# Performance work log

Hardware: AMD Instinct MI355X
Metric: run time of the kernel (lower is better)

## Reference

```python
import jax, jax.numpy as jnp
import numpy as np

N = 200000   # nodes
E = 6400000  # edges
F = 128      # input node features
H = 6        # hiddenSize (module constant)
C = 10       # num_classes
G = 64       # graphs in batch


def setup_inputs() -> dict:
    key = jax.random.key(0)
    ks = jax.random.split(key, 7)
    x = jax.random.normal(ks[0], (N, F), dtype=jnp.float32)
    edge_index = jax.random.randint(ks[1], (2, E), 0, N, dtype=jnp.int32)
    batch = jnp.sort(jax.random.randint(ks[2], (N,), 0, G, dtype=jnp.int32))
    W1 = jax.random.normal(ks[3], (F, H), dtype=jnp.float32) * (1.0 / np.sqrt(F))
    b1 = jnp.zeros((H,), dtype=jnp.float32)
    W2 = jax.random.normal(ks[4], (H, C), dtype=jnp.float32) * (1.0 / np.sqrt(H))
    b2 = jnp.zeros((C,), dtype=jnp.float32)
    return {"x": x, "edge_index": edge_index, "batch": batch,
            "W1": W1, "b1": b1, "W2": W2, "b2": b2}


def _gcn_conv(x, W, b, row, col, dis):
    # PyG GCNConv: h = x W; out = D^{-1/2}(A+I)D^{-1/2} h + b
    h = x @ W                                      # [N, out]
    norm = dis[row] * dis[col]                     # [E] edge normalization
    msg = norm[:, None] * h[row]                   # gather from source nodes
    agg = jax.ops.segment_sum(msg, col, num_segments=N)  # scatter-add to targets
    # self-loop term: norm = dis[i]*dis[i]
    return agg + (dis * dis)[:, None] * h + b


def reference(x, edge_index, batch, W1, b1, W2, b2):
    row, col = edge_index[0], edge_index[1]
    # degree after adding self-loops (edge_weight = 1)
    deg = jax.ops.segment_sum(jnp.ones((E,), dtype=x.dtype), col, num_segments=N) + 1.0
    dis = jax.lax.rsqrt(deg)                       # deg^{-1/2}

    h = _gcn_conv(x, W1, b1, row, col, dis)
    h = jax.nn.relu(h)
    # dropout is identity in inference mode
    h = _gcn_conv(h, W2, b2, row, col, dis)        # [N, C]

    # global mean pool over each graph
    sums = jax.ops.segment_sum(h, batch, num_segments=G)                  # [G, C]
    cnts = jax.ops.segment_sum(jnp.ones((N,), dtype=h.dtype), batch, num_segments=G)
    pooled = sums / jnp.maximum(cnts, 1.0)[:, None]
    return jax.nn.log_softmax(pooled, axis=1)      # [G, C]
```

## Files before the change

### kernel.cpp

```cpp
#include <hip/hip_runtime.h>
#include <math.h>

#define N_NODES 200000
#define N_EDGES 6400000
#define F_IN    128
#define H_HID   6
#define C_OUT   10
#define G_BATCH 64

#define TILE_E  16384
#define NT      ((N_EDGES + TILE_E - 1) / TILE_E)
#define NBUCK   ((N_NODES + 1023) / 1024)
#define BCAP    36864
#define EPT     (TILE_E / 512)
#define QCAP    10240

__device__ __forceinline__ unsigned short f2bf(float f) {
    unsigned u = __float_as_uint(f);
    u += 0x7fff + ((u >> 16) & 1);
    return (unsigned short)(u >> 16);
}
__device__ __forceinline__ unsigned pack2(float a, float b) {
    return (unsigned)f2bf(a) | ((unsigned)f2bf(b) << 16);
}
__device__ __forceinline__ float bf_lo(unsigned u) { return __uint_as_float(u << 16); }
__device__ __forceinline__ float bf_hi(unsigned u) { return __uint_as_float(u & 0xffff0000u); }

__global__ __launch_bounds__(512) void scatterA_kernel(const int* __restrict__ row,
                                                       const int* __restrict__ col,
                                                       int* __restrict__ gcur,
                                                       int* __restrict__ binned, int E) {
    __shared__ int sortbuf[TILE_E];
    __shared__ int cnt[256];
    __shared__ int pos[257];
    __shared__ int cur[256];
    __shared__ int lbase[256];
    int t = blockIdx.x, tid = threadIdx.x;
    int base = t * TILE_E;
    int tile_n = min(TILE_E, E - base);

    if (tid < 256) cnt[tid] = 0;
    __syncthreads();

    int myval[EPT];
#pragma unroll
    for (int k = 0; k < EPT; ++k) {
        int e = base + k * 512 + tid;
        if (e < E) {
            int c = col[e];
            myval[k] = ((c & 1023) << 18) | row[e];
            atomicAdd(&cnt[c >> 10], 1);
        }
    }
    __syncthreads();

    if (tid < 256) pos[tid] = cnt[tid];
    __syncthreads();
    for (int off = 1; off < 256; off <<= 1) {
        int tv = (tid < 256 && tid >= off) ? pos[tid - off] : 0;
        __syncthreads();
        if (tid < 256) pos[tid] += tv;
        __syncthreads();
    }
    int incl = (tid < 256) ? pos[tid] : 0;
    __syncthreads();
    if (tid < 256) {
        int excl = incl - cnt[tid];
        pos[tid] = excl;
        cur[tid] = excl;
        if (tid == 255) pos[256] = incl;
        if (tid < NBUCK) {
            int c = cnt[tid];
            lbase[tid] = tid * BCAP + (c ? atomicAdd(&gcur[tid], c) : 0);
        }
    }
    __syncthreads();

#pragma unroll
    for (int k = 0; k < EPT; ++k) {
        int e = base + k * 512 + tid;
        if (e < E) {
            int b = col[e] >> 10;
            int p = atomicAdd(&cur[b], 1);
            sortbuf[p] = myval[k];
        }
    }
    __syncthreads();

    for (int i = tid; i < tile_n; i += 512) {
        int lo = 0, hi = NBUCK - 1;
        while (lo < hi) {
            int mid = (lo + hi + 1) >> 1;
            if (pos[mid] <= i) lo = mid; else hi = mid - 1;
        }
        binned[lbase[lo] + (i - pos[lo])] = sortbuf[i];
    }
}

__global__ __launch_bounds__(1024) void passB_kernel(const int* __restrict__ gcur,
                                                     const int* __restrict__ binned,
                                                     int* __restrict__ offs, int* __restrict__ endo,
                                                     float* __restrict__ dis,
                                                     int* __restrict__ csr, int E) {
    __shared__ int cnt[1024];
    __shared__ int scn[1024];
    __shared__ int cur[256];
    __shared__ int sortbuf[QCAP];
    int b = blockIdx.x, tid = threadIdx.x;
    int bb = b * BCAP;
    int be = bb + gcur[b];
    cnt[tid] = 0;
    __syncthreads();
    int e = bb + tid;
    for (; e + 3072 < be; e += 4096) {
        int p0 = binned[e], p1 = binned[e + 1024], p2 = binned[e + 2048], p3 = binned[e + 3072];
        atomicAdd(&cnt[p0 >> 18], 1); atomicAdd(&cnt[p1 >> 18], 1);
        atomicAdd(&cnt[p2 >> 18], 1); atomicAdd(&cnt[p3 >> 18], 1);
    }
    for (; e < be; e += 1024) atomicAdd(&cnt[binned[e] >> 18], 1);
    __syncthreads();
    int v = cnt[tid];
    scn[tid] = v;
    __syncthreads();
    for (int off = 1; off < 1024; off <<= 1) {
        int t2 = (tid >= off) ? scn[tid - off] : 0;
        __syncthreads();
        scn[tid] += t2;
        __syncthreads();
    }
    int excl = scn[tid] - v;
    scn[tid] = excl;
    int n = (b << 10) + tid;
    if (n < N_NODES) {
        offs[n] = bb + excl;
        endo[n] = bb + excl + v;
        dis[n] = rsqrtf((float)v + 1.0f);
    }
    __syncthreads();
    int total = be - bb;
#define PLACE(p) { int loc = (p) >> 18; if ((loc >> 8) == q) {                      \
        int ps = scn[loc] - qbase + atomicAdd(&cur[loc & 255], 1);                  \
        if (ps < QCAP) sortbuf[ps] = (p) & 0x3FFFF;                                 \
        else csr[bb + qbase + ps] = (p) & 0x3FFFF; } }
    for (int q = 0; q < 4; ++q) {
        int qbase = scn[q << 8];
        int qend = (q < 3) ? scn[(q + 1) << 8] : total;
        int qn = qend - qbase;
        if (tid < 256) cur[tid] = 0;
        __syncthreads();
        int e2 = bb + tid;
        for (; e2 + 3072 < be; e2 += 4096) {
            int p0 = binned[e2], p1 = binned[e2 + 1024], p2 = binned[e2 + 2048], p3 = binned[e2 + 3072];
            PLACE(p0) PLACE(p1) PLACE(p2) PLACE(p3)
        }
        for (; e2 < be; e2 += 1024) { int p = binned[e2]; PLACE(p) }
        __syncthreads();
        int lim = qn < QCAP ? qn : QCAP;
        for (int i = tid; i < lim; i += 1024) csr[bb + qbase + i] = sortbuf[i];
        __syncthreads();
    }
#undef PLACE
}

__global__ void xw1_kernel(const float* __restrict__ x, const float* __restrict__ W1,
                           const float* __restrict__ dis, uint4* __restrict__ h1b) {
    __shared__ float w[F_IN * H_HID];
    for (int i = threadIdx.x; i < F_IN * H_HID; i += blockDim.x) w[i] = W1[i];
    __syncthreads();
    int n = blockIdx.x * blockDim.x + threadIdx.x;
    if (n >= N_NODES) return;
    float acc[H_HID] = {0.f, 0.f, 0.f, 0.f, 0.f, 0.f};
    const float4* xr = (const float4*)(x + (size_t)n * F_IN);
#pragma unroll 4
    for (int f4 = 0; f4 < F_IN / 4; ++f4) {
        float4 v = xr[f4];
        int f = f4 * 4;
#pragma unroll
        for (int j = 0; j < H_HID; ++j) {
            acc[j] += v.x * w[(f + 0) * H_HID + j] + v.y * w[(f + 1) * H_HID + j]
                    + v.z * w[(f + 2) * H_HID + j] + v.w * w[(f + 3) * H_HID + j];
        }
    }
    float d = dis[n];
    uint4 o;
    o.x = pack2(d * acc[0], d * acc[1]);
    o.y = pack2(d * acc[2], d * acc[3]);
    o.z = pack2(d * acc[4], d * acc[5]);
    o.w = __float_as_uint(d);
    h1b[n] = o;
}

__global__ void gather1_kernel(const int* __restrict__ offs, const int* __restrict__ endo,
                               const int* __restrict__ csr,
                               const uint4* __restrict__ h1b, const float* __restrict__ b1,
                               uint4* __restrict__ rs) {
    int grp = threadIdx.x >> 3, sub = threadIdx.x & 7;
    int n = blockIdx.x * 32 + grp;
    int s = offs[n], e_end = endo[n];
    float a[H_HID] = {0.f, 0.f, 0.f, 0.f, 0.f, 0.f};
    int e = s + sub;
    for (; e + 24 < e_end; e += 32) {
        int i0 = csr[e], i1 = csr[e + 8], i2 = csr[e + 16], i3 = csr[e + 24];
        uint4 v0 = h1b[i0], v1 = h1b[i1], v2 = h1b[i2], v3 = h1b[i3];
        a[0] += (bf_lo(v0.x) + bf_lo(v1.x)) + (bf_lo(v2.x) + bf_lo(v3.x));
        a[1] += (bf_hi(v0.x) + bf_hi(v1.x)) + (bf_hi(v2.x) + bf_hi(v3.x));
        a[2] += (bf_lo(v0.y) + bf_lo(v1.y)) + (bf_lo(v2.y) + bf_lo(v3.y));
        a[3] += (bf_hi(v0.y) + bf_hi(v1.y)) + (bf_hi(v2.y) + bf_hi(v3.y));
        a[4] += (bf_lo(v0.z) + bf_lo(v1.z)) + (bf_lo(v2.z) + bf_lo(v3.z));
        a[5] += (bf_hi(v0.z) + bf_hi(v1.z)) + (bf_hi(v2.z) + bf_hi(v3.z));
    }
    for (; e < e_end; e += 8) {
        uint4 v = h1b[csr[e]];
        a[0] += bf_lo(v.x); a[1] += bf_hi(v.x);
        a[2] += bf_lo(v.y); a[3] += bf_hi(v.y);
        a[4] += bf_lo(v.z); a[5] += bf_hi(v.z);
    }
#pragma unroll
    for (int j = 0; j < H_HID; ++j)
#pragma unroll
        for (int off = 4; off > 0; off >>= 1) a[j] += __shfl_xor(a[j], off);
    uint4 self = h1b[n];
    float d = __uint_as_float(self.w);
    float sf[H_HID] = {bf_lo(self.x), bf_hi(self.x), bf_lo(self.y),
                       bf_hi(self.y), bf_lo(self.z), bf_hi(self.z)};
    if (sub == 0) {
        float r[H_HID];
#pragma unroll
        for (int j = 0; j < H_HID; ++j) {
            float vv = d * (a[j] + sf[j]) + b1[j];
            r[j] = d * (vv > 0.f ? vv : 0.f);
        }
        uint4 o;
        o.x = pack2(r[0], r[1]);
        o.y = pack2(r[2], r[3]);
        o.z = pack2(r[4], r[5]);
        o.w = self.w;
        rs[n] = o;
    }
}

__global__ void gather2_pool_kernel(const int* __restrict__ offs, const int* __restrict__ endo,
                                    const int* __restrict__ csr,
                                    const uint4* __restrict__ rs, const float* __restrict__ W2,
                                    const int* __restrict__ batch, float* __restrict__ sums) {
    __shared__ float w2s[H_HID * C_OUT];
    __shared__ float nodeval[32][C_OUT];
    __shared__ int lg[32];
    if (threadIdx.x < H_HID * C_OUT) w2s[threadIdx.x] = W2[threadIdx.x];
    __syncthreads();
    int grp = threadIdx.x >> 3, sub = threadIdx.x & 7;
    int n = blockIdx.x * 32 + grp;
    int s = offs[n], e_end = endo[n];
    float a[H_HID] = {0.f, 0.f, 0.f, 0.f, 0.f, 0.f};
    int e = s + sub;
    for (; e + 24 < e_end; e += 32) {
        int i0 = csr[e], i1 = csr[e + 8], i2 = csr[e + 16], i3 = csr[e + 24];
        uint4 v0 = rs[i0], v1 = rs[i1], v2 = rs[i2], v3 = rs[i3];
        a[0] += (bf_lo(v0.x) + bf_lo(v1.x)) + (bf_lo(v2.x) + bf_lo(v3.x));
        a[1] += (bf_hi(v0.x) + bf_hi(v1.x)) + (bf_hi(v2.x) + bf_hi(v3.x));
        a[2] += (bf_lo(v0.y) + bf_lo(v1.y)) + (bf_lo(v2.y) + bf_lo(v3.y));
        a[3] += (bf_hi(v0.y) + bf_hi(v1.y)) + (bf_hi(v2.y) + bf_hi(v3.y));
        a[4] += (bf_lo(v0.z) + bf_lo(v1.z)) + (bf_lo(v2.z) + bf_lo(v3.z));
        a[5] += (bf_hi(v0.z) + bf_hi(v1.z)) + (bf_hi(v2.z) + bf_hi(v3.z));
    }
    for (; e < e_end; e += 8) {
        uint4 v = rs[csr[e]];
        a[0] += bf_lo(v.x); a[1] += bf_hi(v.x);
        a[2] += bf_lo(v.y); a[3] += bf_hi(v.y);
        a[4] += bf_lo(v.z); a[5] += bf_hi(v.z);
    }
#pragma unroll
    for (int j = 0; j < H_HID; ++j)
#pragma unroll
        for (int off = 4; off > 0; off >>= 1) a[j] += __shfl_xor(a[j], off);
    uint4 self = rs[n];
    float d = __uint_as_float(self.w);
    float t[H_HID] = {a[0] + bf_lo(self.x), a[1] + bf_hi(self.x), a[2] + bf_lo(self.y),
                      a[3] + bf_hi(self.y), a[4] + bf_lo(self.z), a[5] + bf_hi(self.z)};
    {
        float acc = 0.f;
#pragma unroll
        for (int j = 0; j < H_HID; ++j) acc += t[j] * w2s[j * C_OUT + sub];
        nodeval[grp][sub] = d * acc;
        if (sub < 2) {
            float acc2 = 0.f;
#pragma unroll
            for (int j = 0; j < H_HID; ++j) acc2 += t[j] * w2s[j * C_OUT + sub + 8];
            nodeval[grp][sub + 8] = d * acc2;
        }
    }
    if (sub == 0) lg[grp] = batch[n];
    __syncthreads();
    if (threadIdx.x < C_OUT) {
        int c = threadIdx.x;
        float acc = 0.f;
        int gcur2 = lg[0];
#pragma unroll
        for (int w = 0; w < 32; ++w) {
            if (lg[w] != gcur2) {
                atomicAdd(&sums[gcur2 * C_OUT + c], acc);
                gcur2 = lg[w]; acc = 0.f;
            }
            acc += nodeval[w][c];
        }
        atomicAdd(&sums[gcur2 * C_OUT + c], acc);
    }
}

__global__ void pool_finish_kernel(const float* __restrict__ sums, const int* __restrict__ batch,
                                   const float* __restrict__ b2, float* __restrict__ out) {
    int g = threadIdx.x;
    if (g >= G_BATCH) return;
    int lo = 0, hi = N_NODES;
    while (lo < hi) { int mid = (lo + hi) >> 1; if (batch[mid] < g) lo = mid + 1; else hi = mid; }
    int c0 = lo;
    hi = N_NODES;
    while (lo < hi) { int mid = (lo + hi) >> 1; if (batch[mid] < g + 1) lo = mid + 1; else hi = mid; }
    float inv = 1.0f / fmaxf((float)(lo - c0), 1.0f);
    float v[C_OUT], m = -INFINITY;
#pragma unroll
    for (int c = 0; c < C_OUT; ++c) {
        v[c] = sums[g * C_OUT + c] * inv + b2[c];
        m = fmaxf(m, v[c]);
    }
    float s = 0.f;
#pragma unroll
    for (int c = 0; c < C_OUT; ++c) s += expf(v[c] - m);
    float lse = m + logf(s);
#pragma unroll
    for (int c = 0; c < C_OUT; ++c) out[g * C_OUT + c] = v[c] - lse;
}

extern "C" void kernel_launch(void* const* d_in, const int* in_sizes, int n_in,
                              void* d_out, int out_size, void* d_ws, size_t ws_size,
                              hipStream_t stream) {
    const float* x   = (const float*)d_in[0];
    const int* ei    = (const int*)d_in[1];
    const int* row   = ei;
    const int* col   = ei + N_EDGES;
    const int* batch = (const int*)d_in[2];
    const float* W1  = (const float*)d_in[3];
    const float* b1  = (const float*)d_in[4];
    const float* W2  = (const float*)d_in[5];
    const float* b2  = (const float*)d_in[6];
    float* out = (float*)d_out;

    char* p = (char*)d_ws;
    float* sums   = (float*)p;  p += (size_t)G_BATCH * C_OUT * 4;
    int*   gcur   = (int*)p;    p += (size_t)200 * 4;
    int*   offs   = (int*)p;    p += (size_t)N_NODES * 4;
    int*   endo   = (int*)p;    p += (size_t)N_NODES * 4;
    float* dis    = (float*)p;  p += (size_t)N_NODES * 4;
    int*   csr    = (int*)p;    p += (size_t)NBUCK * BCAP * 4;
    int*   binned = (int*)p;
    uint4* h1b    = (uint4*)binned;
    uint4* rs     = (uint4*)binned + N_NODES;

    hipMemsetAsync(sums, 0, (size_t)G_BATCH * C_OUT * 4 + 200 * 4, stream);

    scatterA_kernel<<<NT, 512, 0, stream>>>(row, col, gcur, binned, N_EDGES);
    passB_kernel   <<<NBUCK, 1024, 0, stream>>>(gcur, binned, offs, endo, dis, csr, N_EDGES);
    xw1_kernel     <<<(N_NODES + 255) / 256, 256, 0, stream>>>(x, W1, dis, h1b);
    gather1_kernel <<<N_NODES / 32, 256, 0, stream>>>(offs, endo, csr, h1b, b1, rs);
    gather2_pool_kernel<<<N_NODES / 32, 256, 0, stream>>>(offs, endo, csr, rs, W2, batch, sums);
    pool_finish_kernel <<<1, 64, 0, stream>>>(sums, batch, b2, out);
}
```

Before: 383.7 us.

## Replace CSR build with bucketed LDS atomic aggregation over 512-node bins

Drops the second sorting pass that turned bucketed edges into a per-node CSR. Both aggregation layers now run one block per 512-node bucket, gathering source features and adding them into per-bucket accumulators in shared memory with atomics. Degrees come from global atomics in the scatter pass, and the rsqrt normalisation is folded into the feature transform. This saves a full edge pass and the CSR arrays, but adds heavy LDS atomic contention (six float atomics per edge) and global degree atomics, and makes the summation order nondeterministic.

```diff
diff --git a/kernel.cpp b/kernel.cpp
--- a/kernel.cpp
+++ b/kernel.cpp
@@ -10,10 +10,11 @@
 
 #define TILE_E  16384
 #define NT      ((N_EDGES + TILE_E - 1) / TILE_E)
-#define NBUCK   ((N_NODES + 1023) / 1024)
-#define BCAP    36864
 #define EPT     (TILE_E / 512)
-#define QCAP    10240
+#define BSH     9
+#define BNODES  512
+#define NBUCK   ((N_NODES + BNODES - 1) / BNODES)
+#define BCAP    18432
 
 __device__ __forceinline__ unsigned short f2bf(float f) {
     unsigned u = __float_as_uint(f);
@@ -29,17 +30,18 @@
 __global__ __launch_bounds__(512) void scatterA_kernel(const int* __restrict__ row,
                                                        const int* __restrict__ col,
                                                        int* __restrict__ gcur,
+                                                       int* __restrict__ deg,
                                                        int* __restrict__ binned, int E) {
     __shared__ int sortbuf[TILE_E];
-    __shared__ int cnt[256];
-    __shared__ int pos[257];
-    __shared__ int cur[256];
-    __shared__ int lbase[256];
+    __shared__ int cnt[512];
+    __shared__ int pos[513];
+    __shared__ int cur[512];
+    __shared__ int lbase[512];
     int t = blockIdx.x, tid = threadIdx.x;
     int base = t * TILE_E;
     int tile_n = min(TILE_E, E - base);
 
-    if (tid < 256) cnt[tid] = 0;
+    cnt[tid] = 0;
     __syncthreads();
 
     int myval[EPT];
@@ -48,27 +50,28 @@
         int e = base + k * 512 + tid;
         if (e < E) {
             int c = col[e];
-            myval[k] = ((c & 1023) << 18) | row[e];
-            atomicAdd(&cnt[c >> 10], 1);
-        }
-    }
-    __syncthreads();
-
-    if (tid < 256) pos[tid] = cnt[tid];
-    __syncthreads();
-    for (int off = 1; off < 256; off <<= 1) {
-        int tv = (tid < 256 && tid >= off) ? pos[tid - off] : 0;
+            myval[k] = ((c & (BNODES - 1)) << 18) | row[e];
+            atomicAdd(&cnt[c >> BSH], 1);
+            atomicAdd(&deg[c], 1);
+        }
+    }
+    __syncthreads();
+
+    pos[tid] = cnt[tid];
+    __syncthreads();
+    for (int off = 1; off < 512; off <<= 1) {
+        int tv = (tid >= off) ? pos[tid - off] : 0;
         __syncthreads();
-        if (tid < 256) pos[tid] += tv;
+        pos[tid] += tv;
         __syncthreads();
     }
-    int incl = (tid < 256) ? pos[tid] : 0;
-    __syncthreads();
-    if (tid < 256) {
+    int incl = pos[tid];
+    __syncthreads();
+    {
         int excl = incl - cnt[tid];
         pos[tid] = excl;
         cur[tid] = excl;
-        if (tid == 255) pos[256] = incl;
+        if (tid == 511) pos[512] = incl;
         if (tid < NBUCK) {
             int c = cnt[tid];
             lbase[tid] = tid * BCAP + (c ? atomicAdd(&gcur[tid], c) : 0);
@@ -80,7 +83,7 @@
     for (int k = 0; k < EPT; ++k) {
         int e = base + k * 512 + tid;
         if (e < E) {
-            int b = col[e] >> 10;
+            int b = col[e] >> BSH;
             int p = atomicAdd(&cur[b], 1);
             sortbuf[p] = myval[k];
         }
@@ -97,73 +100,8 @@
     }
 }
 
-__global__ __launch_bounds__(1024) void passB_kernel(const int* __restrict__ gcur,
-                                                     const int* __restrict__ binned,
-                                                     int* __restrict__ offs, int* __restrict__ endo,
-                                                     float* __restrict__ dis,
-                                                     int* __restrict__ csr, int E) {
-    __shared__ int cnt[1024];
-    __shared__ int scn[1024];
-    __shared__ int cur[256];
-    __shared__ int sortbuf[QCAP];
-    int b = blockIdx.x, tid = threadIdx.x;
-    int bb = b * BCAP;
-    int be = bb + gcur[b];
-    cnt[tid] = 0;
-    __syncthreads();
-    int e = bb + tid;
-    for (; e + 3072 < be; e += 4096) {
-        int p0 = binned[e], p1 = binned[e + 1024], p2 = binned[e + 2048], p3 = binned[e + 3072];
-        atomicAdd(&cnt[p0 >> 18], 1); atomicAdd(&cnt[p1 >> 18], 1);
-        atomicAdd(&cnt[p2 >> 18], 1); atomicAdd(&cnt[p3 >> 18], 1);
-    }
-    for (; e < be; e += 1024) atomicAdd(&cnt[binned[e] >> 18], 1);
-    __syncthreads();
-    int v = cnt[tid];
-    scn[tid] = v;
-    __syncthreads();
-    for (int off = 1; off < 1024; off <<= 1) {
-        int t2 = (tid >= off) ? scn[tid - off] : 0;
-        __syncthreads();
-        scn[tid] += t2;
-        __syncthreads();
-    }
-    int excl = scn[tid] - v;
-    scn[tid] = excl;
-    int n = (b << 10) + tid;
-    if (n < N_NODES) {
-        offs[n] = bb + excl;
-        endo[n] = bb + excl + v;
-        dis[n] = rsqrtf((float)v + 1.0f);
-    }
-    __syncthreads();
-    int total = be - bb;
-#define PLACE(p) { int loc = (p) >> 18; if ((loc >> 8) == q) {                      \
-        int ps = scn[loc] - qbase + atomicAdd(&cur[loc & 255], 1);                  \
-        if (ps < QCAP) sortbuf[ps] = (p) & 0x3FFFF;                                 \
-        else csr[bb + qbase + ps] = (p) & 0x3FFFF; } }
-    for (int q = 0; q < 4; ++q) {
-        int qbase = scn[q << 8];
-        int qend = (q < 3) ? scn[(q + 1) << 8] : total;
-        int qn = qend - qbase;
-        if (tid < 256) cur[tid] = 0;
-        __syncthreads();
-        int e2 = bb + tid;
-        for (; e2 + 3072 < be; e2 += 4096) {
-            int p0 = binned[e2], p1 = binned[e2 + 1024], p2 = binned[e2 + 2048], p3 = binned[e2 + 3072];
-            PLACE(p0) PLACE(p1) PLACE(p2) PLACE(p3)
-        }
-        for (; e2 < be; e2 += 1024) { int p = binned[e2]; PLACE(p) }
-        __syncthreads();
-        int lim = qn < QCAP ? qn : QCAP;
-        for (int i = tid; i < lim; i += 1024) csr[bb + qbase + i] = sortbuf[i];
-        __syncthreads();
-    }
-#undef PLACE
-}
-
 __global__ void xw1_kernel(const float* __restrict__ x, const float* __restrict__ W1,
-                           const float* __restrict__ dis, uint4* __restrict__ h1b) {
+                           const int* __restrict__ deg, uint4* __restrict__ h1b) {
     __shared__ float w[F_IN * H_HID];
     for (int i = threadIdx.x; i < F_IN * H_HID; i += blockDim.x) w[i] = W1[i];
     __syncthreads();
@@ -181,7 +119,7 @@
                     + v.z * w[(f + 2) * H_HID + j] + v.w * w[(f + 3) * H_HID + j];
         }
     }
-    float d = dis[n];
+    float d = rsqrtf((float)deg[n] + 1.0f);
     uint4 o;
     o.x = pack2(d * acc[0], d * acc[1]);
     o.y = pack2(d * acc[2], d * acc[3]);
@@ -190,44 +128,47 @@
     h1b[n] = o;
 }
 
-__global__ void gather1_kernel(const int* __restrict__ offs, const int* __restrict__ endo,
-                               const int* __restrict__ csr,
-                               const uint4* __restrict__ h1b, const float* __restrict__ b1,
-                               uint4* __restrict__ rs) {
-    int grp = threadIdx.x >> 3, sub = threadIdx.x & 7;
-    int n = blockIdx.x * 32 + grp;
-    int s = offs[n], e_end = endo[n];
-    float a[H_HID] = {0.f, 0.f, 0.f, 0.f, 0.f, 0.f};
-    int e = s + sub;
-    for (; e + 24 < e_end; e += 32) {
-        int i0 = csr[e], i1 = csr[e + 8], i2 = csr[e + 16], i3 = csr[e + 24];
-        uint4 v0 = h1b[i0], v1 = h1b[i1], v2 = h1b[i2], v3 = h1b[i3];
-        a[0] += (bf_lo(v0.x) + bf_lo(v1.x)) + (bf_lo(v2.x) + bf_lo(v3.x));
-        a[1] += (bf_hi(v0.x) + bf_hi(v1.x)) + (bf_hi(v2.x) + bf_hi(v3.x));
-        a[2] += (bf_lo(v0.y) + bf_lo(v1.y)) + (bf_lo(v2.y) + bf_lo(v3.y));
-        a[3] += (bf_hi(v0.y) + bf_hi(v1.y)) + (bf_hi(v2.y) + bf_hi(v3.y));
-        a[4] += (bf_lo(v0.z) + bf_lo(v1.z)) + (bf_lo(v2.z) + bf_lo(v3.z));
-        a[5] += (bf_hi(v0.z) + bf_hi(v1.z)) + (bf_hi(v2.z) + bf_hi(v3.z));
-    }
-    for (; e < e_end; e += 8) {
-        uint4 v = h1b[csr[e]];
-        a[0] += bf_lo(v.x); a[1] += bf_hi(v.x);
-        a[2] += bf_lo(v.y); a[3] += bf_hi(v.y);
-        a[4] += bf_lo(v.z); a[5] += bf_hi(v.z);
-    }
-#pragma unroll
-    for (int j = 0; j < H_HID; ++j)
-#pragma unroll
-        for (int off = 4; off > 0; off >>= 1) a[j] += __shfl_xor(a[j], off);
-    uint4 self = h1b[n];
-    float d = __uint_as_float(self.w);
-    float sf[H_HID] = {bf_lo(self.x), bf_hi(self.x), bf_lo(self.y),
-                       bf_hi(self.y), bf_lo(self.z), bf_hi(self.z)};
-    if (sub == 0) {
+#define EDGE_ACC(v, l)                                                  \
+    atomicAdd(&acc[0][l], bf_lo(v.x)); atomicAdd(&acc[1][l], bf_hi(v.x)); \
+    atomicAdd(&acc[2][l], bf_lo(v.y)); atomicAdd(&acc[3][l], bf_hi(v.y)); \
+    atomicAdd(&acc[4][l], bf_lo(v.z)); atomicAdd(&acc[5][l], bf_hi(v.z));
+
+__global__ __launch_bounds__(512) void agg1_kernel(const int* __restrict__ gcur,
+                                                   const int* __restrict__ binned,
+                                                   const uint4* __restrict__ h1b,
+                                                   const float* __restrict__ b1,
+                                                   uint4* __restrict__ rs) {
+    __shared__ float acc[H_HID][BNODES];
+    int b = blockIdx.x, tid = threadIdx.x;
+#pragma unroll
+    for (int j = 0; j < H_HID; ++j) acc[j][tid] = 0.f;
+    __syncthreads();
+    int bb = b * BCAP, be = bb + gcur[b];
+    int e = bb + tid;
+    for (; e + 1536 < be; e += 2048) {
+        int p0 = binned[e], p1 = binned[e + 512], p2 = binned[e + 1024], p3 = binned[e + 1536];
+        uint4 v0 = h1b[p0 & 0x3FFFF], v1 = h1b[p1 & 0x3FFFF],
+              v2 = h1b[p2 & 0x3FFFF], v3 = h1b[p3 & 0x3FFFF];
+        int l0 = p0 >> 18, l1 = p1 >> 18, l2 = p2 >> 18, l3 = p3 >> 18;
+        EDGE_ACC(v0, l0) EDGE_ACC(v1, l1) EDGE_ACC(v2, l2) EDGE_ACC(v3, l3)
+    }
+    for (; e < be; e += 512) {
+        int p = binned[e];
+        uint4 v = h1b[p & 0x3FFFF];
+        int l = p >> 18;
+        EDGE_ACC(v, l)
+    }
+    __syncthreads();
+    int n = b * BNODES + tid;
+    if (n < N_NODES) {
+        uint4 self = h1b[n];
+        float d = __uint_as_float(self.w);
+        float sf[H_HID] = {bf_lo(self.x), bf_hi(self.x), bf_lo(self.y),
+                           bf_hi(self.y), bf_lo(self.z), bf_hi(self.z)};
         float r[H_HID];
 #pragma unroll
         for (int j = 0; j < H_HID; ++j) {
-            float vv = d * (a[j] + sf[j]) + b1[j];
+            float vv = d * (acc[j][tid] + sf[j]) + b1[j];
             r[j] = d * (vv > 0.f ? vv : 0.f);
         }
         uint4 o;
@@ -239,71 +180,71 @@
     }
 }
 
-__global__ void gather2_pool_kernel(const int* __restrict__ offs, const int* __restrict__ endo,
-                                    const int* __restrict__ csr,
-                                    const uint4* __restrict__ rs, const float* __restrict__ W2,
-                                    const int* __restrict__ batch, float* __restrict__ sums) {
+__global__ __launch_bounds__(512) void agg2_pool_kernel(const int* __restrict__ gcur,
+                                                        const int* __restrict__ binned,
+                                                        const uint4* __restrict__ rs,
+                                                        const float* __restrict__ W2,
+                                                        const int* __restrict__ batch,
+                                                        float* __restrict__ sums) {
+    __shared__ float acc[H_HID][BNODES];
     __shared__ float w2s[H_HID * C_OUT];
-    __shared__ float nodeval[32][C_OUT];
-    __shared__ int lg[32];
-    if (threadIdx.x < H_HID * C_OUT) w2s[threadIdx.x] = W2[threadIdx.x];
-    __syncthreads();
-    int grp = threadIdx.x >> 3, sub = threadIdx.x & 7;
-    int n = blockIdx.x * 32 + grp;
-    int s = offs[n], e_end = endo[n];
-    float a[H_HID] = {0.f, 0.f, 0.f, 0.f, 0.f, 0.f};
-    int e = s + sub;
-    for (; e + 24 < e_end; e += 32) {
-        int i0 = csr[e], i1 = csr[e + 8], i2 = csr[e + 16], i3 = csr[e + 24];
-        uint4 v0 = rs[i0], v1 = rs[i1], v2 = rs[i2], v3 = rs[i3];
-        a[0] += (bf_lo(v0.x) + bf_lo(v1.x)) + (bf_lo(v2.x) + bf_lo(v3.x));
-        a[1] += (bf_hi(v0.x) + bf_hi(v1.x)) + (bf_hi(v2.x) + bf_hi(v3.x));
-        a[2] += (bf_lo(v0.y) + bf_lo(v1.y)) + (bf_lo(v2.y) + bf_lo(v3.y));
-        a[3] += (bf_hi(v0.y) + bf_hi(v1.y)) + (bf_hi(v2.y) + bf_hi(v3.y));
-        a[4] += (bf_lo(v0.z) + bf_lo(v1.z)) + (bf_lo(v2.z) + bf_lo(v3.z));
-        a[5] += (bf_hi(v0.z) + bf_hi(v1.z)) + (bf_hi(v2.z) + bf_hi(v3.z));
-    }
-    for (; e < e_end; e += 8) {
-        uint4 v = rs[csr[e]];
-        a[0] += bf_lo(v.x); a[1] += bf_hi(v.x);
-        a[2] += bf_lo(v.y); a[3] += bf_hi(v.y);
-        a[4] += bf_lo(v.z); a[5] += bf_hi(v.z);
-    }
-#pragma unroll
-    for (int j = 0; j < H_HID; ++j)
-#pragma unroll
-        for (int off = 4; off > 0; off >>= 1) a[j] += __shfl_xor(a[j], off);
-    uint4 self = rs[n];
-    float d = __uint_as_float(self.w);
-    float t[H_HID] = {a[0] + bf_lo(self.x), a[1] + bf_hi(self.x), a[2] + bf_lo(self.y),
-                      a[3] + bf_hi(self.y), a[4] + bf_lo(self.z), a[5] + bf_hi(self.z)};
-    {
-        float acc = 0.f;
-#pragma unroll
-        for (int j = 0; j < H_HID; ++j) acc += t[j] * w2s[j * C_OUT + sub];
-        nodeval[grp][sub] = d * acc;
-        if (sub < 2) {
-            float acc2 = 0.f;
-#pragma unroll
-            for (int j = 0; j < H_HID; ++j) acc2 += t[j] * w2s[j * C_OUT + sub + 8];
-            nodeval[grp][sub + 8] = d * acc2;
-        }
-    }
-    if (sub == 0) lg[grp] = batch[n];
-    __syncthreads();
-    if (threadIdx.x < C_OUT) {
-        int c = threadIdx.x;
-        float acc = 0.f;
-        int gcur2 = lg[0];
-#pragma unroll
-        for (int w = 0; w < 32; ++w) {
-            if (lg[w] != gcur2) {
-                atomicAdd(&sums[gcur2 * C_OUT + c], acc);
-                gcur2 = lg[w]; acc = 0.f;
+    __shared__ float nv[BNODES][C_OUT + 1];
+    __shared__ int lg[BNODES];
+    int b = blockIdx.x, tid = threadIdx.x;
+#pragma unroll
+    for (int j = 0; j < H_HID; ++j) acc[j][tid] = 0.f;
+    if (tid < H_HID * C_OUT) w2s[tid] = W2[tid];
+    __syncthreads();
+    int bb = b * BCAP, be = bb + gcur[b];
+    int e = bb + tid;
+    for (; e + 1536 < be; e += 2048) {
+        int p0 = binned[e], p1 = binned[e + 512], p2 = binned[e + 1024], p3 = binned[e + 1536];
+        uint4 v0 = rs[p0 & 0x3FFFF], v1 = rs[p1 & 0x3FFFF],
+              v2 = rs[p2 & 0x3FFFF], v3 = rs[p3 & 0x3FFFF];
+        int l0 = p0 >> 18, l1 = p1 >> 18, l2 = p2 >> 18, l3 = p3 >> 18;
+        EDGE_ACC(v0, l0) EDGE_ACC(v1, l1) EDGE_ACC(v2, l2) EDGE_ACC(v3, l3)
+    }
+    for (; e < be; e += 512) {
+        int p = binned[e];
+        uint4 v = rs[p & 0x3FFFF];
+        int l = p >> 18;
+        EDGE_ACC(v, l)
+    }
+    __syncthreads();
+    int n = b * BNODES + tid;
+    if (n < N_NODES) {
+        uint4 self = rs[n];
+        float d = __uint_as_float(self.w);
+        float t0 = acc[0][tid] + bf_lo(self.x), t1 = acc[1][tid] + bf_hi(self.x),
+              t2 = acc[2][tid] + bf_lo(self.y), t3 = acc[3][tid] + bf_hi(self.y),
+              t4 = acc[4][tid] + bf_lo(self.z), t5 = acc[5][tid] + bf_hi(self.z);
+#pragma unroll
+        for (int c = 0; c < C_OUT; ++c) {
+            float a2 = t0 * w2s[c]             + t1 * w2s[C_OUT + c]
+                     + t2 * w2s[2 * C_OUT + c] + t3 * w2s[3 * C_OUT + c]
+                     + t4 * w2s[4 * C_OUT + c] + t5 * w2s[5 * C_OUT + c];
+            nv[tid][c] = d * a2;
+        }
+        lg[tid] = batch[n];
+    } else {
+#pragma unroll
+        for (int c = 0; c < C_OUT; ++c) nv[tid][c] = 0.f;
+        lg[tid] = G_BATCH - 1;
+    }
+    __syncthreads();
+    if (tid < 80) {
+        int seg = tid / 10, c = tid - seg * 10;
+        int g = -1; float a2 = 0.f;
+        for (int ii = 0; ii < 64; ++ii) {
+            int w = (seg << 6) + ((ii + 9 * seg) & 63);
+            int gw = lg[w];
+            if (gw != g) {
+                if (g >= 0) atomicAdd(&sums[g * C_OUT + c], a2);
+                g = gw; a2 = 0.f;
             }
-            acc += nodeval[w][c];
-        }
-        atomicAdd(&sums[gcur2 * C_OUT + c], acc);
+            a2 += nv[w][c];
+        }
+        atomicAdd(&sums[g * C_OUT + c], a2);
     }
 }
 
@@ -347,21 +288,18 @@
 
     char* p = (char*)d_ws;
     float* sums   = (float*)p;  p += (size_t)G_BATCH * C_OUT * 4;
-    int*   gcur   = (int*)p;    p += (size_t)200 * 4;
-    int*   offs   = (int*)p;    p += (size_t)N_NODES * 4;
-    int*   endo   = (int*)p;    p += (size_t)N_NODES * 4;
-    float* dis    = (float*)p;  p += (size_t)N_NODES * 4;
-    int*   csr    = (int*)p;    p += (size_t)NBUCK * BCAP * 4;
-    int*   binned = (int*)p;
-    uint4* h1b    = (uint4*)binned;
-    uint4* rs     = (uint4*)binned + N_NODES;
-
-    hipMemsetAsync(sums, 0, (size_t)G_BATCH * C_OUT * 4 + 200 * 4, stream);
-
-    scatterA_kernel<<<NT, 512, 0, stream>>>(row, col, gcur, binned, N_EDGES);
-    passB_kernel   <<<NBUCK, 1024, 0, stream>>>(gcur, binned, offs, endo, dis, csr, N_EDGES);
-    xw1_kernel     <<<(N_NODES + 255) / 256, 256, 0, stream>>>(x, W1, dis, h1b);
-    gather1_kernel <<<N_NODES / 32, 256, 0, stream>>>(offs, endo, csr, h1b, b1, rs);
-    gather2_pool_kernel<<<N_NODES / 32, 256, 0, stream>>>(offs, endo, csr, rs, W2, batch, sums);
-    pool_finish_kernel <<<1, 64, 0, stream>>>(sums, batch, b2, out);
-}
+    int*   gcur   = (int*)p;    p += (size_t)400 * 4;
+    int*   deg    = (int*)p;    p += (size_t)N_NODES * 4;
+    int*   binned = (int*)p;    p += (size_t)NBUCK * BCAP * 4;
+    uint4* h1b    = (uint4*)p;  p += (size_t)N_NODES * 16;
+    uint4* rs     = (uint4*)p;
+
+    hipMemsetAsync(sums, 0,
+                   (size_t)G_BATCH * C_OUT * 4 + 400 * 4 + (size_t)N_NODES * 4, stream);
+
+    scatterA_kernel<<<NT, 512, 0, stream>>>(row, col, gcur, deg, binned, N_EDGES);
+    xw1_kernel     <<<(N_NODES + 255) / 256, 256, 0, stream>>>(x, W1, deg, h1b);
+    agg1_kernel    <<<NBUCK, 512, 0, stream>>>(gcur, binned, h1b, b1, rs);
+    agg2_pool_kernel<<<NBUCK, 512, 0, stream>>>(gcur, binned, rs, W2, batch, sums);
+    pool_finish_kernel<<<1, 64, 0, stream>>>(sums, batch, b2, out);
+}
```

After: 1.000 ms. 2.61x slower.
